# Kernel tuning notes

Measured on AMD Instinct MI355X. Metric: run time of the kernel, lower is better.

## Reference

```python
import jax, jax.numpy as jnp
import numpy as np

B, T, C = 2, 2048, 2048
NH, NKVH = 16, 4
HS = C // NH  # 128
NEG_INF = -1e30


def _rope_freqs(T, hs, base=10000.0):
    inv = 1.0 / (base ** (np.arange(0, hs, 2, dtype=np.float32) / hs))  # [hs/2]
    ang = np.arange(T, dtype=np.float32)[:, None] * inv[None, :]        # [T, hs/2]
    return jnp.asarray(np.cos(ang)), jnp.asarray(np.sin(ang))


def setup_inputs() -> dict:
    key = jax.random.key(0)
    ks = jax.random.split(key, 4)
    x = jax.random.normal(ks[0], (B, T, C), dtype=jnp.float32)
    W_attn = jax.random.normal(ks[1], (C, C + 2 * NKVH * HS), dtype=jnp.float32) * 0.02
    b_attn = jnp.zeros((C + 2 * NKVH * HS,), dtype=jnp.float32)
    W_proj = jax.random.normal(ks[2], (C, C), dtype=jnp.float32) * 0.02
    b_proj = jnp.zeros((C,), dtype=jnp.float32)
    freqs_cos, freqs_sin = _rope_freqs(T, HS)
    return {"x": x, "freqs_cos": freqs_cos, "freqs_sin": freqs_sin,
            "W_attn": W_attn, "b_attn": b_attn, "W_proj": W_proj, "b_proj": b_proj}


def _apply_rope(x, cos, sin):
    # x: [B, T, H, hs]; cos/sin: [T, hs/2] -> broadcast [1, T, 1, hs/2]
    b, t, h, hs = x.shape
    x_ = x.reshape(b, t, h, hs // 2, 2)
    re, im = x_[..., 0], x_[..., 1]
    c = cos[None, :, None, :]
    s = sin[None, :, None, :]
    out_re = re * c - im * s
    out_im = re * s + im * c
    return jnp.stack([out_re, out_im], axis=-1).reshape(b, t, h, hs)


def reference(x, freqs_cos, freqs_sin, W_attn, b_attn, W_proj, b_proj):
    b, t, c = x.shape
    qkv = x @ W_attn + b_attn                                   # [B,T,C+2*nkvh*hs]
    q, k, v = jnp.split(qkv, [c, c + NKVH * HS], axis=2)
    q = q.reshape(b, t, NH, HS)
    k = k.reshape(b, t, NKVH, HS)
    v = v.reshape(b, t, NKVH, HS)
    q = _apply_rope(q, freqs_cos, freqs_sin)
    k = _apply_rope(k, freqs_cos, freqs_sin)
    # group heads: q [B, nkvh, rep, T, hs]; k,v [B, nkvh, T, hs]
    rep = NH // NKVH
    q = q.transpose(0, 2, 1, 3).reshape(b, NKVH, rep, t, HS)
    k = k.transpose(0, 2, 1, 3)
    v = v.transpose(0, 2, 1, 3)
    scale = 1.0 / jnp.sqrt(jnp.asarray(HS, dtype=x.dtype))
    scores = jnp.einsum('bgrth,bgsh->bgrts', q, k) * scale      # [B,g,rep,T,T]
    causal = jnp.tril(jnp.ones((t, t), dtype=bool))
    scores = jnp.where(causal[None, None, None], scores, NEG_INF)
    att = jax.nn.softmax(scores, axis=-1)
    y = jnp.einsum('bgrts,bgsh->bgrth', att, v)                 # [B,g,rep,T,hs]
    y = y.reshape(b, NH, t, HS).transpose(0, 2, 1, 3).reshape(b, t, c)
    return y @ W_proj + b_proj
```

## Files before the change

### kernel.cpp

```cpp
#include <hip/hip_runtime.h>
#include <hip/hip_bf16.h>
#include <stdint.h>

#define B_ 2
#define T_ 2048
#define C_ 2048
#define NH_ 16
#define NKVH_ 4
#define HS_ 128
#define QKV_ 3072
#define NTOK_ 4096

typedef __attribute__((ext_vector_type(4))) float f32x4;
typedef __attribute__((ext_vector_type(16))) float f32x16;
typedef __attribute__((ext_vector_type(8))) short s16x8;

__device__ __forceinline__ short f2bf(float f) {
    union { float f; unsigned u; } v; v.f = f;
    unsigned r = v.u + 0x7FFFu + ((v.u >> 16) & 1u);
    return (short)(r >> 16);
}

__device__ __forceinline__ void async16(const void* g, void* l) {
    __builtin_amdgcn_global_load_lds(
        (const __attribute__((address_space(1))) void*)g,
        (__attribute__((address_space(3))) void*)l, 16, 0, 0);
}

__global__ void cast_bf16_kernel(const float* __restrict__ x, short* __restrict__ out, int n8) {
    int i = blockIdx.x * 256 + threadIdx.x;
    if (i >= n8) return;
    const float4* p = (const float4*)x + (size_t)i * 2;
    float4 a = p[0], b = p[1];
    short o[8] = { f2bf(a.x), f2bf(a.y), f2bf(a.z), f2bf(a.w),
                   f2bf(b.x), f2bf(b.y), f2bf(b.z), f2bf(b.w) };
    *(int4*)(out + (size_t)i * 8) = *(const int4*)o;
}

__global__ void transcast(const float* __restrict__ W, short* __restrict__ WT, int Kd, int Nd) {
    __shared__ float tile[64][65];
    int k0 = blockIdx.x * 64, n0 = blockIdx.y * 64;
    int tid = threadIdx.x;
    int cl = tid & 63, rw = tid >> 6;
    for (int it = 0; it < 16; ++it) {
        int r = it * 4 + rw;
        tile[r][cl] = W[(size_t)(k0 + r) * Nd + n0 + cl];
    }
    __syncthreads();
    for (int it = 0; it < 16; ++it) {
        int n = it * 4 + rw;
        WT[(size_t)(n0 + n) * Kd + k0 + cl] = f2bf(tile[cl][n]);
    }
}

__global__ __launch_bounds__(256, 2) void gemm_bt(
    const short* __restrict__ A, const short* __restrict__ Bt,
    const float* __restrict__ bias, float* __restrict__ Cc,
    int M, int N, int K)
{
    __shared__ short As[128 * 64];
    __shared__ short Bs[128 * 64];
    int tid = threadIdx.x;
    int w = tid >> 6, l = tid & 63;
    int lr = l & 15, lg = l >> 4;
    int bm = blockIdx.x, bn = blockIdx.y;
    int wm = (w >> 1) * 64, wn = (w & 1) * 64;
    f32x4 acc[4][4];
#pragma unroll
    for (int i = 0; i < 4; i++)
#pragma unroll
        for (int j = 0; j < 4; j++) { acc[i][j][0]=0.f; acc[i][j][1]=0.f; acc[i][j][2]=0.f; acc[i][j][3]=0.f; }
    int arow = l >> 3, acol = (l & 7) * 8;
    for (int k0 = 0; k0 < K; k0 += 64) {
#pragma unroll
        for (int i = 0; i < 4; i++) {
            int chunk = w * 4 + i;
            int row = chunk * 8 + arow;
            async16(A  + (size_t)(bm * 128 + row) * K + k0 + acol, (char*)As + chunk * 1024);
            async16(Bt + (size_t)(bn * 128 + row) * K + k0 + acol, (char*)Bs + chunk * 1024);
        }
        __syncthreads();
#pragma unroll
        for (int ks = 0; ks < 2; ks++) {
            s16x8 af[4], bf[4];
#pragma unroll
            for (int mi = 0; mi < 4; mi++)
                af[mi] = *(const s16x8*)&As[(wm + mi * 16 + lr) * 64 + ks * 32 + lg * 8];
#pragma unroll
            for (int ni = 0; ni < 4; ni++)
                bf[ni] = *(const s16x8*)&Bs[(wn + ni * 16 + lr) * 64 + ks * 32 + lg * 8];
#pragma unroll
            for (int mi = 0; mi < 4; mi++)
#pragma unroll
                for (int ni = 0; ni < 4; ni++)
                    acc[mi][ni] = __builtin_amdgcn_mfma_f32_16x16x32_bf16(af[mi], bf[ni], acc[mi][ni], 0, 0, 0);
        }
        __syncthreads();
    }
#pragma unroll
    for (int mi = 0; mi < 4; mi++) {
        int row = bm * 128 + wm + mi * 16 + lg * 4;
#pragma unroll
        for (int ni = 0; ni < 4; ni++) {
            int col = bn * 128 + wn + ni * 16 + lr;
            float bv = bias[col];
#pragma unroll
            for (int j = 0; j < 4; j++)
                Cc[(size_t)(row + j) * N + col] = acc[mi][ni][j] + bv;
        }
    }
}

__global__ void rope_scatter(const float* __restrict__ qkv,
                             const float* __restrict__ fcos, const float* __restrict__ fsin,
                             short* __restrict__ Q, short* __restrict__ Kb)
{
    const float qscale = 0.08838834764831845f;
    int idx = blockIdx.x * 256 + threadIdx.x;
    int tok = idx / 1280, p = idx - tok * 1280;
    if (tok >= NTOK_) return;
    int b = tok >> 11, t = tok & 2047;
    if (p < 1024) {
        int h = p >> 6, i = p & 63;
        const float* src = qkv + (size_t)tok * QKV_ + h * 128 + 2 * i;
        float re = src[0], im = src[1];
        float c = fcos[t * 64 + i], s = fsin[t * 64 + i];
        unsigned lo = (unsigned short)f2bf((re * c - im * s) * qscale);
        unsigned hi = (unsigned short)f2bf((re * s + im * c) * qscale);
        *(unsigned*)(Q + ((size_t)(b * NH_ + h) * T_ + t) * HS_ + 2 * i) = lo | (hi << 16);
    } else {
        int pk = p - 1024; int g = pk >> 6, i = pk & 63;
        const float* src = qkv + (size_t)tok * QKV_ + C_ + g * 128 + 2 * i;
        float re = src[0], im = src[1];
        float c = fcos[t * 64 + i], s = fsin[t * 64 + i];
        unsigned lo = (unsigned short)f2bf(re * c - im * s);
        unsigned hi = (unsigned short)f2bf(re * s + im * c);
        *(unsigned*)(Kb + ((size_t)(b * NKVH_ + g) * T_ + t) * HS_ + 2 * i) = lo | (hi << 16);
    }
}

__global__ void v_transpose(const float* __restrict__ qkv, short* __restrict__ VT) {
    __shared__ float tile[64][65];
    int t0 = blockIdx.x * 64, d0 = blockIdx.y * 64;
    int bg = blockIdx.z; int b = bg >> 2, g = bg & 3;
    int tid = threadIdx.x; int cl = tid & 63, rw = tid >> 6;
    const float* base = qkv + (size_t)(b * T_ + t0) * QKV_ + C_ + NKVH_ * HS_ + g * HS_ + d0;
    for (int it = 0; it < 16; ++it) {
        int r = it * 4 + rw;
        tile[r][cl] = base[(size_t)r * QKV_ + cl];
    }
    __syncthreads();
    short* out = VT + ((size_t)(b * NKVH_ + g) * HS_ + d0) * T_ + t0;
    for (int it = 0; it < 16; ++it) {
        int d = it * 4 + rw;
        out[(size_t)d * T_ + cl] = f2bf(tile[cl][d]);
    }
}

__global__ __launch_bounds__(256, 2) void attn_kernel(
    const short* __restrict__ Qg, const short* __restrict__ Kg,
    const short* __restrict__ VTg, short* __restrict__ Y)
{
    __shared__ short Ks[2][64 * 128];
    __shared__ short VTs[2][128 * 64];
    __shared__ short Ps[4][32 * 64];
    int tid = threadIdx.x, w = tid >> 6, l = tid & 63;
    int l31 = l & 31, hi = l >> 5;
    int qt = 15 - (int)blockIdx.y;
    int bh = blockIdx.x;
    int b = bh >> 4, h = bh & 15, g = h >> 2;
    const short* Qb = Qg + (size_t)(b * NH_ + h) * T_ * HS_;
    const short* Kb = Kg + (size_t)(b * NKVH_ + g) * T_ * HS_;
    const short* Vb = VTg + (size_t)(b * NKVH_ + g) * HS_ * T_;

    auto STAGE = [&](int st, int buf) {
#pragma unroll
        for (int i = 0; i < 4; i++) {
            int chunk = w * 4 + i;
            int poff = chunk * 1024 + l * 16;
            int qoffk = poff ^ (((poff >> 8) & 7) << 4);
            async16(Kb + (size_t)(st * 64 + (qoffk >> 8)) * HS_ + ((qoffk & 255) >> 1),
                    (char*)&Ks[buf][0] + chunk * 1024);
            int qoffv = poff ^ (((poff >> 7) & 7) << 4);
            async16(Vb + (size_t)(qoffv >> 7) * T_ + st * 64 + ((qoffv & 127) >> 1),
                    (char*)&VTs[buf][0] + chunk * 1024);
        }
    };

    int qw = qt * 128 + w * 32;
    int qglob = qw + l31;

    s16x8 qf[8];
#pragma unroll
    for (int dc = 0; dc < 8; dc++)
        qf[dc] = *(const s16x8*)(Qb + (size_t)qglob * HS_ + dc * 16 + hi * 8);

    f32x16 oacc[4];
#pragma unroll
    for (int db = 0; db < 4; db++)
#pragma unroll
        for (int i = 0; i < 16; i++) oacc[db][i] = 0.f;
    float m = -1e30f, lsum = 0.f;
    int nst = 2 * qt + 2;

    STAGE(0, 0);
    __syncthreads();
    int cur = 0;

    for (int st = 0; st < nst; ++st) {
        if (st + 1 < nst) STAGE(st + 1, cur ^ 1);
        if (st * 64 <= qw) {
            const char* KsC = (const char*)&Ks[cur][0];
            const char* VsC = (const char*)&VTs[cur][0];
            char* PsC = (char*)&Ps[w][0];

            f32x16 sacc[2];
#pragma unroll
            for (int sb = 0; sb < 2; sb++) {
                f32x16 a;
#pragma unroll
                for (int i = 0; i < 16; i++) a[i] = 0.f;
#pragma unroll
                for (int dc = 0; dc < 8; dc++) {
                    int lo = (sb * 32 + l31) * 256 + dc * 32 + hi * 16;
                    int po = lo ^ (((lo >> 8) & 7) << 4);
                    s16x8 kf = *(const s16x8*)(KsC + po);
                    a = __builtin_amdgcn_mfma_f32_32x32x16_bf16(kf, qf[dc], a, 0, 0, 0);
                }
                sacc[sb] = a;
            }
            if (st * 64 + 63 > qw) {
#pragma unroll
                for (int sb = 0; sb < 2; sb++)
#pragma unroll
                    for (int r = 0; r < 16; r++) {
                        int s = st * 64 + sb * 32 + (r & 3) + 8 * (r >> 2) + 4 * hi;
                        if (s > qglob) sacc[sb][r] = -1e30f;
                    }
            }
            float tm = -1e30f;
#pragma unroll
            for (int sb = 0; sb < 2; sb++)
#pragma unroll
                for (int r = 0; r < 16; r++) tm = fmaxf(tm, sacc[sb][r]);
            tm = fmaxf(tm, __shfl_xor(tm, 32));
            if (__any(tm > m)) {
                float mn = fmaxf(m, tm);
                float corr = __expf(m - mn);
                m = mn; lsum *= corr;
#pragma unroll
                for (int db = 0; db < 4; db++)
#pragma unroll
                    for (int r = 0; r < 16; r++) oacc[db][r] *= corr;
            }
#pragma unroll
            for (int sb = 0; sb < 2; sb++)
#pragma unroll
                for (int r = 0; r < 16; r++) {
                    float p = __expf(sacc[sb][r] - m);
                    lsum += p;
                    int sl = sb * 32 + (r & 3) + 8 * (r >> 2) + 4 * hi;
                    int lo = l31 * 128 + sl * 2;
                    int po = lo ^ (((lo >> 7) & 7) << 4);
                    *(short*)(PsC + po) = f2bf(p);
                }
#pragma unroll
            for (int sc = 0; sc < 4; sc++) {
                int lp = l31 * 128 + sc * 32 + hi * 16;
                int pp = lp ^ (((lp >> 7) & 7) << 4);
                s16x8 pf = *(const s16x8*)(PsC + pp);
#pragma unroll
                for (int db = 0; db < 4; db++) {
                    int lo = (db * 32 + l31) * 128 + sc * 32 + hi * 16;
                    int po = lo ^ (((lo >> 7) & 7) << 4);
                    s16x8 vf = *(const s16x8*)(VsC + po);
                    oacc[db] = __builtin_amdgcn_mfma_f32_32x32x16_bf16(vf, pf, oacc[db], 0, 0, 0);
                }
            }
        }
        __syncthreads();
        cur ^= 1;
    }

    lsum += __shfl_xor(lsum, 32);
    float inv = 1.0f / lsum;
    short* Yrow = Y + (size_t)(b * T_ + qglob) * C_ + h * 128;
#pragma unroll
    for (int db = 0; db < 4; db++)
#pragma unroll
        for (int pr = 0; pr < 8; pr++) {
            unsigned u0 = (unsigned short)f2bf(oacc[db][2 * pr] * inv);
            unsigned u1 = (unsigned short)f2bf(oacc[db][2 * pr + 1] * inv);
            int d = db * 32 + ((2 * pr) & 3) + 8 * (pr >> 1) + 4 * hi;
            *(unsigned*)(Yrow + d) = u0 | (u1 << 16);
        }
}

extern "C" void kernel_launch(void* const* d_in, const int* in_sizes, int n_in,
                              void* d_out, int out_size, void* d_ws, size_t ws_size,
                              hipStream_t stream)
{
    const float* x      = (const float*)d_in[0];
    const float* fcos   = (const float*)d_in[1];
    const float* fsin   = (const float*)d_in[2];
    const float* W_attn = (const float*)d_in[3];
    const float* b_attn = (const float*)d_in[4];
    const float* W_proj = (const float*)d_in[5];
    const float* b_proj = (const float*)d_in[6];
    float* out = (float*)d_out;
    char* ws = (char*)d_ws;

    short* xb  = (short*)(ws + 0);
    float* qkv = (float*)(ws + 16777216);
    short* y   = (short*)(ws + 16777216);
    short* WpT = (short*)(ws + 33554432);
    short* WaT = (short*)(ws + 67108864);
    short* Qb  = (short*)(ws + 67108864);
    short* Kb  = (short*)(ws + 83886080);
    short* VT  = (short*)(ws + 88080384);

    cast_bf16_kernel<<<4096, 256, 0, stream>>>(x, xb, NTOK_ * C_ / 8);
    transcast<<<dim3(32, 48), 256, 0, stream>>>(W_attn, WaT, C_, QKV_);
    gemm_bt<<<dim3(32, 24), 256, 0, stream>>>(xb, WaT, b_attn, qkv, NTOK_, QKV_, C_);
    rope_scatter<<<20480, 256, 0, stream>>>(qkv, fcos, fsin, Qb, Kb);
    v_transpose<<<dim3(32, 2, 8), 256, 0, stream>>>(qkv, VT);
    transcast<<<dim3(32, 32), 256, 0, stream>>>(W_proj, WpT, C_, C_);
    attn_kernel<<<dim3(32, 16), 256, 0, stream>>>(Qb, Kb, VT, y);
    gemm_bt<<<dim3(32, 16), 256, 0, stream>>>(y, WpT, b_proj, out, NTOK_, C_, C_);
}
```

Before: 225.3 us.

## Read V directly from global memory, split QK accumulators, pack P stores

Drops the LDS staging of the transposed V tile and loads V fragments for the PV MFMAs straight from global memory. The QK^T dot product is split across two independent accumulators to shorten the MFMA dependency chain. Probabilities are packed four at a time into 8-byte stores into a padded P buffer instead of a swizzled one. This frees LDS and removes the async V copies, but each wave now issues uncached, latency-exposed global loads per tile, and several waves and blocks re-read the same V data.

Result: slower. 266.1 us (+18.1%).

```diff
diff --git a/kernel.cpp b/kernel.cpp
--- a/kernel.cpp
+++ b/kernel.cpp
@@ -162,8 +162,7 @@
     const short* __restrict__ VTg, short* __restrict__ Y)
 {
     __shared__ short Ks[2][64 * 128];
-    __shared__ short VTs[2][128 * 64];
-    __shared__ short Ps[4][32 * 64];
+    __shared__ short Ps[4][32 * 68];
     int tid = threadIdx.x, w = tid >> 6, l = tid & 63;
     int l31 = l & 31, hi = l >> 5;
     int qt = 15 - (int)blockIdx.y;
@@ -181,9 +180,6 @@
             int qoffk = poff ^ (((poff >> 8) & 7) << 4);
             async16(Kb + (size_t)(st * 64 + (qoffk >> 8)) * HS_ + ((qoffk & 255) >> 1),
                     (char*)&Ks[buf][0] + chunk * 1024);
-            int qoffv = poff ^ (((poff >> 7) & 7) << 4);
-            async16(Vb + (size_t)(qoffv >> 7) * T_ + st * 64 + ((qoffv & 127) >> 1),
-                    (char*)&VTs[buf][0] + chunk * 1024);
         }
     };
 
@@ -211,23 +207,28 @@
         if (st + 1 < nst) STAGE(st + 1, cur ^ 1);
         if (st * 64 <= qw) {
             const char* KsC = (const char*)&Ks[cur][0];
-            const char* VsC = (const char*)&VTs[cur][0];
             char* PsC = (char*)&Ps[w][0];
 
             f32x16 sacc[2];
 #pragma unroll
             for (int sb = 0; sb < 2; sb++) {
-                f32x16 a;
-#pragma unroll
-                for (int i = 0; i < 16; i++) a[i] = 0.f;
-#pragma unroll
-                for (int dc = 0; dc < 8; dc++) {
-                    int lo = (sb * 32 + l31) * 256 + dc * 32 + hi * 16;
-                    int po = lo ^ (((lo >> 8) & 7) << 4);
-                    s16x8 kf = *(const s16x8*)(KsC + po);
-                    a = __builtin_amdgcn_mfma_f32_32x32x16_bf16(kf, qf[dc], a, 0, 0, 0);
+                f32x16 a0, a1;
+#pragma unroll
+                for (int i = 0; i < 16; i++) { a0[i] = 0.f; a1[i] = 0.f; }
+#pragma unroll
+                for (int dc = 0; dc < 4; dc++) {
+                    int lo0 = (sb * 32 + l31) * 256 + dc * 32 + hi * 16;
+                    int po0 = lo0 ^ (((lo0 >> 8) & 7) << 4);
+                    s16x8 kf0 = *(const s16x8*)(KsC + po0);
+                    a0 = __builtin_amdgcn_mfma_f32_32x32x16_bf16(kf0, qf[dc], a0, 0, 0, 0);
+                    int lo1 = (sb * 32 + l31) * 256 + (dc + 4) * 32 + hi * 16;
+                    int po1 = lo1 ^ (((lo1 >> 8) & 7) << 4);
+                    s16x8 kf1 = *(const s16x8*)(KsC + po1);
+                    a1 = __builtin_amdgcn_mfma_f32_32x32x16_bf16(kf1, qf[dc + 4], a1, 0, 0, 0);
                 }
-                sacc[sb] = a;
+#pragma unroll
+                for (int i = 0; i < 16; i++) a0[i] += a1[i];
+                sacc[sb] = a0;
             }
             if (st * 64 + 63 > qw) {
 #pragma unroll
@@ -256,24 +257,29 @@
 #pragma unroll
             for (int sb = 0; sb < 2; sb++)
 #pragma unroll
-                for (int r = 0; r < 16; r++) {
-                    float p = __expf(sacc[sb][r] - m);
-                    lsum += p;
-                    int sl = sb * 32 + (r & 3) + 8 * (r >> 2) + 4 * hi;
-                    int lo = l31 * 128 + sl * 2;
-                    int po = lo ^ (((lo >> 7) & 7) << 4);
-                    *(short*)(PsC + po) = f2bf(p);
+                for (int k = 0; k < 4; k++) {
+                    float p0 = __expf(sacc[sb][4 * k]     - m);
+                    float p1 = __expf(sacc[sb][4 * k + 1] - m);
+                    float p2 = __expf(sacc[sb][4 * k + 2] - m);
+                    float p3 = __expf(sacc[sb][4 * k + 3] - m);
+                    lsum += (p0 + p1) + (p2 + p3);
+                    unsigned w01 = (unsigned short)f2bf(p0) | ((unsigned)(unsigned short)f2bf(p1) << 16);
+                    unsigned w23 = (unsigned short)f2bf(p2) | ((unsigned)(unsigned short)f2bf(p3) << 16);
+                    uint2 pkv; pkv.x = w01; pkv.y = w23;
+                    int sl = sb * 32 + 8 * k + 4 * hi;
+                    *(uint2*)(PsC + l31 * 136 + sl * 2) = pkv;
                 }
 #pragma unroll
             for (int sc = 0; sc < 4; sc++) {
-                int lp = l31 * 128 + sc * 32 + hi * 16;
-                int pp = lp ^ (((lp >> 7) & 7) << 4);
-                s16x8 pf = *(const s16x8*)(PsC + pp);
+                unsigned ptmp[4];
+                const char* pb = PsC + l31 * 136 + (sc * 16 + hi * 8) * 2;
+                *(uint2*)&ptmp[0] = *(const uint2*)pb;
+                *(uint2*)&ptmp[2] = *(const uint2*)(pb + 8);
+                s16x8 pf = *(const s16x8*)ptmp;
 #pragma unroll
                 for (int db = 0; db < 4; db++) {
-                    int lo = (db * 32 + l31) * 128 + sc * 32 + hi * 16;
-                    int po = lo ^ (((lo >> 7) & 7) << 4);
-                    s16x8 vf = *(const s16x8*)(VsC + po);
+                    s16x8 vf = *(const s16x8*)(Vb + (size_t)(db * 32 + l31) * T_
+                                               + st * 64 + sc * 16 + hi * 8);
                     oacc[db] = __builtin_amdgcn_mfma_f32_32x32x16_bf16(vf, pf, oacc[db], 0, 0, 0);
                 }
             }
```
